# Kernel tuning notes

Measured on AMD Instinct MI355X. Metric: run time of the kernel, lower is better.

Reference implementation:

```python
import jax, jax.numpy as jnp
import numpy as np

N = 100000      # nodes
E = 1600000     # edges
F_IN = 128
F_HID = 128
F_OUT = 40
BN_EPS = 1e-5


def gcn_layer(x, W, b, src, dst):
    # PyG GCNConv with default gcn_norm: add self-loops, symmetric deg^-1/2 norm.
    h = x @ W                                   # [N, F_out] dense transform first (F_out <= F_in friendly)
    loop = jnp.arange(N)
    s = jnp.concatenate([src, loop])            # [E+N] sources incl. self-loops
    d = jnp.concatenate([dst, loop])            # [E+N] targets incl. self-loops
    deg = jax.ops.segment_sum(jnp.ones(s.shape, dtype=h.dtype), d, num_segments=N)
    dinv = jnp.where(deg > 0, jax.lax.rsqrt(deg), jnp.zeros((), h.dtype))
    norm = dinv[s] * dinv[d]                    # [E+N]
    out = jax.ops.segment_sum(h[s] * norm[:, None], d, num_segments=N)
    return out + b


def setup_inputs() -> dict:
    key = jax.random.key(0)
    ks = jax.random.split(key, 8)
    x = jax.random.normal(ks[0], (N, F_IN), dtype=jnp.float32)
    edge_src = jax.random.randint(ks[1], (E,), 0, N)
    edge_dst = jax.random.randint(ks[2], (E,), 0, N)
    W1 = jax.random.normal(ks[3], (F_IN, F_HID), dtype=jnp.float32) * (1.0 / np.sqrt(F_IN))
    b1 = jnp.zeros((F_HID,), dtype=jnp.float32)
    gamma = jnp.ones((F_HID,), dtype=jnp.float32)
    beta = jnp.zeros((F_HID,), dtype=jnp.float32)
    W2 = jax.random.normal(ks[4], (F_HID, F_OUT), dtype=jnp.float32) * (1.0 / np.sqrt(F_HID))
    b2 = jnp.zeros((F_OUT,), dtype=jnp.float32)
    return {"x": x, "W1": W1, "b1": b1, "gamma": gamma, "beta": beta,
            "W2": W2, "b2": b2, "edge_src": edge_src, "edge_dst": edge_dst}


def reference(x, W1, b1, gamma, beta, W2, b2, edge_src, edge_dst):
    h = gcn_layer(x, W1, b1, edge_src, edge_dst)            # GCNConv 1
    mean = jnp.mean(h, axis=0)                               # BatchNorm1d (batch stats, deterministic)
    var = jnp.mean(jnp.square(h - mean), axis=0)
    h = (h - mean) * jax.lax.rsqrt(var + BN_EPS) * gamma + beta
    h = jax.nn.relu(h)                                       # ReLU; dropout is identity (eval/deterministic)
    h = gcn_layer(h, W2, b2, edge_src, edge_dst)            # GCNConv 2
    return jax.nn.log_softmax(h, axis=1)
```

## Files before the change

### kernel.cpp

```cpp
#include <hip/hip_runtime.h>
#include <cstdint>
#include <cstddef>

constexpr int N_NODES = 100000;
constexpr int N_EDGES = 1600000;
constexpr int F_IN   = 128;
constexpr int F_HID  = 128;
constexpr int F_OUT  = 40;
constexpr float BN_EPS = 1e-5f;

constexpr int NBUCK  = 196;
constexpr int ECHUNK = 4096;
constexpr int NCHUNK = (N_EDGES + ECHUNK - 1) / ECHUNK;
constexpr int BCAP   = 16384;

typedef unsigned int uint;
typedef unsigned short ushort;
typedef __attribute__((ext_vector_type(8))) short short8v;
typedef __attribute__((ext_vector_type(4))) float f32x4;

__device__ inline uint bf16_rne(float f) {
    uint u = __float_as_uint(f);
    return (u + 0x7fffu + ((u >> 16) & 1u)) >> 16;
}
__device__ inline float bf_lo(uint u) { return __uint_as_float(u << 16); }
__device__ inline float bf_hi(uint u) { return __uint_as_float(u & 0xffff0000u); }

__global__ __launch_bounds__(256) void k_wcast(const float* __restrict__ W1,
                                               const float* __restrict__ W2,
                                               ushort* __restrict__ w1b,
                                               ushort* __restrict__ w2b,
                                               int* __restrict__ gfill,
                                               float* __restrict__ bnsum,
                                               float* __restrict__ bnsq) {
    int i = blockIdx.x * 256 + threadIdx.x;
    if (i < NBUCK) gfill[i] = 0;
    if (i < 128) { bnsum[i] = 0.f; bnsq[i] = 0.f; }
    if (i < 128 * 128) {
        int n = i >> 7, k = i & 127;
        w1b[i] = (ushort)bf16_rne(W1[k * 128 + n]);
    }
    if (i < 48 * 128) {
        int c = i >> 7, k = i & 127;
        w2b[i] = (c < F_OUT) ? (ushort)bf16_rne(W2[k * F_OUT + c]) : (ushort)0;
    }
}

__global__ __launch_bounds__(256) void k_part(const int* __restrict__ src,
                                              const int* __restrict__ dst,
                                              int* __restrict__ gfill,
                                              uint* __restrict__ ebuf) {
    __shared__ uint pk[ECHUNK];
    __shared__ uint gd[ECHUNK];
    __shared__ int hist[NBUCK], loff[NBUCK], gpos[NBUCK], lfill[NBUCK];
    __shared__ int sc[256];
    int t = threadIdx.x;
    for (int i = t; i < NBUCK; i += 256) { hist[i] = 0; lfill[i] = 0; }
    __syncthreads();
    int base = blockIdx.x * ECHUNK;
    int n = min(ECHUNK, N_EDGES - base);
    for (int i = t; i < n; i += 256)
        atomicAdd(&hist[dst[base + i] >> 9], 1);
    __syncthreads();
    int c = (t < NBUCK) ? hist[t] : 0;
    sc[t] = c;
    __syncthreads();
    #pragma unroll
    for (int o = 1; o < 256; o <<= 1) {
        int v = (t >= o) ? sc[t - o] : 0;
        __syncthreads();
        sc[t] += v;
        __syncthreads();
    }
    if (t < NBUCK) {
        loff[t] = sc[t] - c;
        gpos[t] = c ? atomicAdd(&gfill[t], c) : 0;
    }
    __syncthreads();
    for (int i = t; i < n; i += 256) {
        int d = dst[base + i];
        int s2 = src[base + i];
        int b = d >> 9;
        int lp = atomicAdd(&lfill[b], 1);
        int idx = loff[b] + lp;
        int off = gpos[b] + lp;
        pk[idx] = (uint)s2 | ((uint)(d & 511) << 17);
        gd[idx] = (off < BCAP) ? (uint)(b * BCAP + off) : 0xFFFFFFFFu;
    }
    __syncthreads();
    for (int i = t; i < n; i += 256) {
        uint g = gd[i];
        if (g != 0xFFFFFFFFu) ebuf[g] = pk[i];
    }
}

__global__ __launch_bounds__(256) void k_csr(const uint* __restrict__ ebuf,
                                             const int* __restrict__ gfill,
                                             int* __restrict__ rowptr,
                                             int* __restrict__ rowend,
                                             float* __restrict__ dinv,
                                             int* __restrict__ colidx) {
    __shared__ int hist[512];
    __shared__ int lptr[512];
    int t = threadIdx.x;
    int b = blockIdx.x;
    int v0 = b << 9;
    int e0 = b * BCAP;
    int m = min(gfill[b], BCAP);
    for (int i = t; i < 512; i += 256) hist[i] = 0;
    __syncthreads();
    for (int i = t; i < m; i += 256)
        atomicAdd(&hist[ebuf[e0 + i] >> 17], 1);
    __syncthreads();
    if (t < 64) {
        int run = 0;
        #pragma unroll
        for (int j = 0; j < 8; ++j) { lptr[8 * t + j] = run; run += hist[8 * t + j]; }
        int inc = run;
        #pragma unroll
        for (int o = 1; o < 64; o <<= 1) {
            int u = __shfl_up(inc, o);
            if (t >= o) inc += u;
        }
        int excl = inc - run;
        #pragma unroll
        for (int j = 0; j < 8; ++j) lptr[8 * t + j] += excl;
    }
    __syncthreads();
    for (int i = t; i < 512; i += 256) {
        int v = v0 + i;
        if (v < N_NODES) {
            int beg = e0 + lptr[i];
            rowptr[v] = beg;
            rowend[v] = beg + hist[i];
            dinv[v] = rsqrtf((float)(hist[i] + 1));
        }
    }
    __syncthreads();
    for (int i = t; i < 512; i += 256) hist[i] = 0;
    __syncthreads();
    for (int i = t; i < m; i += 256) {
        uint p = ebuf[e0 + i];
        int lr = (int)(p >> 17);
        int lp = atomicAdd(&hist[lr], 1);
        colidx[e0 + lptr[lr] + lp] = (int)(p & 0x1FFFFu);
    }
}

__global__ __launch_bounds__(256) void k_gemm1(const float* __restrict__ x,
                                               const ushort* __restrict__ w1b,
                                               const float* __restrict__ dinv,
                                               uint* __restrict__ h1b) {
    __shared__ float sm[64 * 132];
    int wid = threadIdx.x >> 6, lane = threadIdx.x & 63;
    int li = lane & 15, kg = lane >> 4;
    int row = blockIdx.x * 64 + wid * 16 + li;
    int rc = min(row, N_NODES - 1);
    const float* xr = x + (size_t)rc * 128;
    f32x4 acc[8] = {};
    #pragma unroll
    for (int kk = 0; kk < 4; ++kk) {
        int k0 = kk * 32 + kg * 8;
        float4 xv0 = *(const float4*)(xr + k0);
        float4 xv1 = *(const float4*)(xr + k0 + 4);
        short8v a;
        a[0] = (short)bf16_rne(xv0.x); a[1] = (short)bf16_rne(xv0.y);
        a[2] = (short)bf16_rne(xv0.z); a[3] = (short)bf16_rne(xv0.w);
        a[4] = (short)bf16_rne(xv1.x); a[5] = (short)bf16_rne(xv1.y);
        a[6] = (short)bf16_rne(xv1.z); a[7] = (short)bf16_rne(xv1.w);
        #pragma unroll
        for (int n = 0; n < 8; ++n) {
            short8v b = *(const short8v*)(w1b + (n * 16 + li) * 128 + k0);
            acc[n] = __builtin_amdgcn_mfma_f32_16x16x32_bf16(a, b, acc[n], 0, 0, 0);
        }
    }
    #pragma unroll
    for (int n = 0; n < 8; ++n)
        #pragma unroll
        for (int j = 0; j < 4; ++j)
            sm[(wid * 16 + kg * 4 + j) * 132 + n * 16 + li] = acc[n][j];
    __syncthreads();
    int rr = threadIdx.x >> 2, cb = (threadIdx.x & 3) * 32;
    int grow = blockIdx.x * 64 + rr;
    if (grow < N_NODES) {
        float dv = dinv[grow];
        const float4* sp4 = (const float4*)(sm + rr * 132 + cb);
        uint4 ov[4];
        #pragma unroll
        for (int q = 0; q < 4; ++q) {
            float4 e0 = sp4[2 * q], e1 = sp4[2 * q + 1];
            ov[q].x = bf16_rne(e0.x * dv) | (bf16_rne(e0.y * dv) << 16);
            ov[q].y = bf16_rne(e0.z * dv) | (bf16_rne(e0.w * dv) << 16);
            ov[q].z = bf16_rne(e1.x * dv) | (bf16_rne(e1.y * dv) << 16);
            ov[q].w = bf16_rne(e1.z * dv) | (bf16_rne(e1.w * dv) << 16);
        }
        uint4* dst = (uint4*)(h1b + (size_t)grow * 64 + cb / 2);
        #pragma unroll
        for (int q = 0; q < 4; ++q) dst[q] = ov[q];
    }
}

__global__ __launch_bounds__(256) void k_agg1(const uint* __restrict__ h1b,
                                              const int* __restrict__ rowptr,
                                              const int* __restrict__ rowend,
                                              const int* __restrict__ colidx,
                                              const float* __restrict__ dinv,
                                              const float* __restrict__ b1,
                                              uint* __restrict__ out1b) {
    const uint4* h1b4 = (const uint4*)h1b;
    int v = __builtin_amdgcn_readfirstlane(blockIdx.x * 4 + (threadIdx.x >> 6));
    if (v >= N_NODES) return;
    int lane = threadIdx.x & 63;
    int g = lane >> 4, c = lane & 15;
    int beg = rowptr[v], end = rowend[v];
    float a0 = 0, a1 = 0, a2 = 0, a3 = 0, a4 = 0, a5 = 0, a6 = 0, a7 = 0;
    #define ACC8(u) { a0 += bf_lo(u.x); a1 += bf_hi(u.x); a2 += bf_lo(u.y); a3 += bf_hi(u.y); \
                      a4 += bf_lo(u.z); a5 += bf_hi(u.z); a6 += bf_lo(u.w); a7 += bf_hi(u.w); }
    if (g == 0) {
        uint4 us = h1b4[(size_t)v * 16 + c];
        ACC8(us);
    }
    int p = beg + g;
    for (; p + 12 < end; p += 16) {
        int s0 = colidx[p], s1 = colidx[p + 4], s2 = colidx[p + 8], s3 = colidx[p + 12];
        uint4 u0 = h1b4[(size_t)s0 * 16 + c];
        uint4 u1 = h1b4[(size_t)s1 * 16 + c];
        uint4 u2 = h1b4[(size_t)s2 * 16 + c];
        uint4 u3 = h1b4[(size_t)s3 * 16 + c];
        ACC8(u0); ACC8(u1); ACC8(u2); ACC8(u3);
    }
    for (; p < end; p += 4) {
        uint4 u = h1b4[(size_t)colidx[p] * 16 + c];
        ACC8(u);
    }
    #undef ACC8
    a0 += __shfl_xor(a0, 16); a0 += __shfl_xor(a0, 32);
    a1 += __shfl_xor(a1, 16); a1 += __shfl_xor(a1, 32);
    a2 += __shfl_xor(a2, 16); a2 += __shfl_xor(a2, 32);
    a3 += __shfl_xor(a3, 16); a3 += __shfl_xor(a3, 32);
    a4 += __shfl_xor(a4, 16); a4 += __shfl_xor(a4, 32);
    a5 += __shfl_xor(a5, 16); a5 += __shfl_xor(a5, 32);
    a6 += __shfl_xor(a6, 16); a6 += __shfl_xor(a6, 32);
    a7 += __shfl_xor(a7, 16); a7 += __shfl_xor(a7, 32);
    if (g == 0) {
        float dv = dinv[v];
        const float* bp = b1 + 8 * c;
        float o0 = fmaf(dv, a0, bp[0]), o1 = fmaf(dv, a1, bp[1]);
        float o2 = fmaf(dv, a2, bp[2]), o3 = fmaf(dv, a3, bp[3]);
        float o4 = fmaf(dv, a4, bp[4]), o5 = fmaf(dv, a5, bp[5]);
        float o6 = fmaf(dv, a6, bp[6]), o7 = fmaf(dv, a7, bp[7]);
        uint4 ov;
        ov.x = bf16_rne(o0) | (bf16_rne(o1) << 16);
        ov.y = bf16_rne(o2) | (bf16_rne(o3) << 16);
        ov.z = bf16_rne(o4) | (bf16_rne(o5) << 16);
        ov.w = bf16_rne(o6) | (bf16_rne(o7) << 16);
        *(uint4*)(out1b + (size_t)v * 64 + 4 * c) = ov;
    }
}

__global__ __launch_bounds__(256) void k_bnstats(const uint* __restrict__ out1b,
                                                 float* __restrict__ sum,
                                                 float* __restrict__ sumsq) {
    int t = threadIdx.x;
    int f = t & 63;
    int r = blockIdx.x * 4 + (t >> 6);
    float s0 = 0, ss0 = 0, s1 = 0, ss1 = 0;
    for (; r < N_NODES; r += gridDim.x * 4) {
        uint u = out1b[(size_t)r * 64 + f];
        float a = bf_lo(u), b = bf_hi(u);
        s0 += a; ss0 += a * a;
        s1 += b; ss1 += b * b;
    }
    __shared__ float ls[256][4];
    ls[t][0] = s0; ls[t][1] = ss0; ls[t][2] = s1; ls[t][3] = ss1;
    __syncthreads();
    if (t < 64) {
        float A = ls[t][0] + ls[t + 64][0] + ls[t + 128][0] + ls[t + 192][0];
        float B = ls[t][1] + ls[t + 64][1] + ls[t + 128][1] + ls[t + 192][1];
        float C = ls[t][2] + ls[t + 64][2] + ls[t + 128][2] + ls[t + 192][2];
        float D = ls[t][3] + ls[t + 64][3] + ls[t + 128][3] + ls[t + 192][3];
        atomicAdd(&sum[2 * f], A);
        atomicAdd(&sumsq[2 * f], B);
        atomicAdd(&sum[2 * f + 1], C);
        atomicAdd(&sumsq[2 * f + 1], D);
    }
}

__global__ __launch_bounds__(256) void k_gemm2(const uint* __restrict__ out1b,
                                               const ushort* __restrict__ w2b,
                                               const float* __restrict__ bnsum,
                                               const float* __restrict__ bnsq,
                                               const float* __restrict__ gamma,
                                               const float* __restrict__ beta,
                                               const float* __restrict__ dinv,
                                               uint* __restrict__ h2f) {
    __shared__ float sm[64 * 52];
    __shared__ float scs[128], shs[128];
    if (threadIdx.x < 128) {
        int f = threadIdx.x;
        float mean = bnsum[f] * (1.f / N_NODES);
        float var = bnsq[f] * (1.f / N_NODES) - mean * mean;
        float rstd = rsqrtf(var + BN_EPS);
        float sc = gamma[f] * rstd;
        scs[f] = sc;
        shs[f] = beta[f] - mean * sc;
    }
    __syncthreads();
    int wid = threadIdx.x >> 6, lane = threadIdx.x & 63;
    int li = lane & 15, kg = lane >> 4;
    int row = blockIdx.x * 64 + wid * 16 + li;
    int rc = min(row, N_NODES - 1);
    const uint* xr = out1b + (size_t)rc * 64;
    f32x4 acc[3] = {};
    #pragma unroll
    for (int kk = 0; kk < 4; ++kk) {
        int k0 = kk * 32 + kg * 8;
        uint4 uv = *(const uint4*)(xr + k0 / 2);
        float4 sc0 = *(const float4*)(scs + k0);
        float4 sc1 = *(const float4*)(scs + k0 + 4);
        float4 sh0 = *(const float4*)(shs + k0);
        float4 sh1 = *(const float4*)(shs + k0 + 4);
        float e0 = fmaxf(fmaf(bf_lo(uv.x), sc0.x, sh0.x), 0.f);
        float e1 = fmaxf(fmaf(bf_hi(uv.x), sc0.y, sh0.y), 0.f);
        float e2 = fmaxf(fmaf(bf_lo(uv.y), sc0.z, sh0.z), 0.f);
        float e3 = fmaxf(fmaf(bf_hi(uv.y), sc0.w, sh0.w), 0.f);
        float e4 = fmaxf(fmaf(bf_lo(uv.z), sc1.x, sh1.x), 0.f);
        float e5 = fmaxf(fmaf(bf_hi(uv.z), sc1.y, sh1.y), 0.f);
        float e6 = fmaxf(fmaf(bf_lo(uv.w), sc1.z, sh1.z), 0.f);
        float e7 = fmaxf(fmaf(bf_hi(uv.w), sc1.w, sh1.w), 0.f);
        short8v a;
        a[0] = (short)bf16_rne(e0); a[1] = (short)bf16_rne(e1);
        a[2] = (short)bf16_rne(e2); a[3] = (short)bf16_rne(e3);
        a[4] = (short)bf16_rne(e4); a[5] = (short)bf16_rne(e5);
        a[6] = (short)bf16_rne(e6); a[7] = (short)bf16_rne(e7);
        #pragma unroll
        for (int n = 0; n < 3; ++n) {
            short8v b = *(const short8v*)(w2b + (n * 16 + li) * 128 + k0);
            acc[n] = __builtin_amdgcn_mfma_f32_16x16x32_bf16(a, b, acc[n], 0, 0, 0);
        }
    }
    #pragma unroll
    for (int n = 0; n < 3; ++n)
        #pragma unroll
        for (int j = 0; j < 4; ++j)
            sm[(wid * 16 + kg * 4 + j) * 52 + n * 16 + li] = acc[n][j];
    __syncthreads();
    int rr = threadIdx.x;
    int grow = blockIdx.x * 64 + rr;
    if (rr < 64 && grow < N_NODES) {
        float dv = dinv[grow];
        const float* sp = sm + rr * 52;
        uint o[10];
        #pragma unroll
        for (int i = 0; i < 10; ++i) {
            int p = 0;
            p = __builtin_amdgcn_cvt_pk_fp8_f32(sp[4 * i] * dv,     sp[4 * i + 1] * dv, p, false);
            p = __builtin_amdgcn_cvt_pk_fp8_f32(sp[4 * i + 2] * dv, sp[4 * i + 3] * dv, p, true);
            o[i] = (uint)p;
        }
        uint4* dst = (uint4*)(h2f + (size_t)grow * 16);
        dst[0] = make_uint4(o[0], o[1], o[2], o[3]);
        dst[1] = make_uint4(o[4], o[5], o[6], o[7]);
        *(uint2*)(h2f + (size_t)grow * 16 + 8) = make_uint2(o[8], o[9]);
    }
}

__global__ __launch_bounds__(256) void k_agg2(const uint* __restrict__ h2f,
                                              const int* __restrict__ rowptr,
                                              const int* __restrict__ rowend,
                                              const int* __restrict__ colidx,
                                              const float* __restrict__ dinv,
                                              const float* __restrict__ b2,
                                              float* __restrict__ out) {
    __shared__ float sm[4][64][4];
    int wid = threadIdx.x >> 6;
    int v = __builtin_amdgcn_readfirstlane(blockIdx.x * 4 + wid);
    if (v >= N_NODES) return;
    int lane = threadIdx.x & 63;
    int g = lane / 10;
    int c = lane - g * 10;
    bool act = g < 6;
    int beg = rowptr[v], end = rowend[v];
    float a0 = 0, a1 = 0, a2 = 0, a3 = 0;
    #define ACC4(u) { auto lo = __builtin_amdgcn_cvt_pk_f32_fp8((int)(u), false); \
                      auto hi = __builtin_amdgcn_cvt_pk_f32_fp8((int)(u), true);  \
                      a0 += lo[0]; a1 += lo[1]; a2 += hi[0]; a3 += hi[1]; }
    if (act) {
        if (g == 0) {
            uint u = h2f[(size_t)v * 16 + c];
            ACC4(u);
        }
        int p = beg + g;
        for (; p + 18 < end; p += 24) {
            int s0 = colidx[p], s1 = colidx[p + 6], s2 = colidx[p + 12], s3 = colidx[p + 18];
            uint u0 = h2f[(size_t)s0 * 16 + c];
            uint u1 = h2f[(size_t)s1 * 16 + c];
            uint u2 = h2f[(size_t)s2 * 16 + c];
            uint u3 = h2f[(size_t)s3 * 16 + c];
            ACC4(u0); ACC4(u1); ACC4(u2); ACC4(u3);
        }
        for (; p < end; p += 6) {
            uint u = h2f[(size_t)colidx[p] * 16 + c];
            ACC4(u);
        }
    }
    #undef ACC4
    float4* slot = (float4*)&sm[wid][lane][0];
    *slot = make_float4(a0, a1, a2, a3);
    asm volatile("s_waitcnt lgkmcnt(0)" ::: "memory");
    __builtin_amdgcn_sched_barrier(0);
    float z = -1e30f;
    if (lane < F_OUT) {
        int cc = lane >> 2, jj = lane & 3;
        float s = sm[wid][cc][jj]      + sm[wid][10 + cc][jj] + sm[wid][20 + cc][jj]
                + sm[wid][30 + cc][jj] + sm[wid][40 + cc][jj] + sm[wid][50 + cc][jj];
        z = fmaf(dinv[v], s, b2[lane]);
    }
    float m = z;
    #pragma unroll
    for (int off = 32; off; off >>= 1) m = fmaxf(m, __shfl_xor(m, off));
    float e = (lane < F_OUT) ? __expf(z - m) : 0.f;
    float ssum = e;
    #pragma unroll
    for (int off = 32; off; off >>= 1) ssum += __shfl_xor(ssum, off);
    if (lane < F_OUT) out[(size_t)v * F_OUT + lane] = z - m - __logf(ssum);
}

extern "C" void kernel_launch(void* const* d_in, const int* in_sizes, int n_in,
                              void* d_out, int out_size, void* d_ws, size_t ws_size,
                              hipStream_t stream) {
    const float* x     = (const float*)d_in[0];
    const float* W1    = (const float*)d_in[1];
    const float* b1    = (const float*)d_in[2];
    const float* gamma = (const float*)d_in[3];
    const float* beta  = (const float*)d_in[4];
    const float* W2    = (const float*)d_in[5];
    const float* b2    = (const float*)d_in[6];
    const int* esrc    = (const int*)d_in[7];
    const int* edst    = (const int*)d_in[8];
    float* out         = (float*)d_out;

    char* w = (char*)d_ws;
    size_t off = 0;
    auto alloc = [&](size_t bytes) -> void* {
        void* p = w + off;
        off = (off + bytes + 255) & ~(size_t)255;
        return p;
    };
    int*   gfill  = (int*)alloc(NBUCK * 4);
    int*   rowptr = (int*)alloc(N_NODES * 4);
    int*   rowend = (int*)alloc(N_NODES * 4);
    float* dinv   = (float*)alloc(N_NODES * 4);
    int*   colidx = (int*)alloc((size_t)NBUCK * BCAP * 4);
    uint*  h1b    = (uint*)alloc((size_t)N_NODES * 64 * 4);
    uint*  out1b  = (uint*)alloc((size_t)N_NODES * 64 * 4);
    uint*  h2f    = (uint*)alloc((size_t)N_NODES * 16 * 4);
    ushort* w1b   = (ushort*)alloc(128 * 128 * 2);
    ushort* w2b   = (ushort*)alloc(48 * 128 * 2);
    float* bnsum  = (float*)alloc(128 * 4);
    float* bnsq   = (float*)alloc(128 * 4);
    uint*  ebuf   = h1b;

    (void)ws_size; (void)in_sizes; (void)n_in; (void)out_size;

    k_wcast<<<64, 256, 0, stream>>>(W1, W2, w1b, w2b, gfill, bnsum, bnsq);

    k_part <<<NCHUNK, 256, 0, stream>>>(esrc, edst, gfill, ebuf);
    k_csr  <<<NBUCK, 256, 0, stream>>>(ebuf, gfill, rowptr, rowend, dinv, colidx);

    k_gemm1<<<(N_NODES + 63) / 64, 256, 0, stream>>>(x, w1b, dinv, h1b);
    k_agg1<<<(N_NODES + 3) / 4, 256, 0, stream>>>(h1b, rowptr, rowend, colidx, dinv, b1, out1b);

    k_bnstats<<<512, 256, 0, stream>>>(out1b, bnsum, bnsq);

    k_gemm2<<<(N_NODES + 63) / 64, 256, 0, stream>>>(out1b, w2b, bnsum, bnsq, gamma, beta, dinv, h2f);
    k_agg2<<<(N_NODES + 3) / 4, 256, 0, stream>>>(h2f, rowptr, rowend, colidx, dinv, b2, out);
}
```

Measured before the change: 255.3 us.

## Widen partition/CSR blocks to 512 threads, wave-scan buckets, split agg1 launch

```diff
diff --git a/kernel.cpp b/kernel.cpp
--- a/kernel.cpp
+++ b/kernel.cpp
@@ -46,38 +46,47 @@
     }
 }
 
-__global__ __launch_bounds__(256) void k_part(const int* __restrict__ src,
+__global__ __launch_bounds__(512) void k_part(const int* __restrict__ src,
                                               const int* __restrict__ dst,
                                               int* __restrict__ gfill,
                                               uint* __restrict__ ebuf) {
     __shared__ uint pk[ECHUNK];
     __shared__ uint gd[ECHUNK];
     __shared__ int hist[NBUCK], loff[NBUCK], gpos[NBUCK], lfill[NBUCK];
-    __shared__ int sc[256];
     int t = threadIdx.x;
-    for (int i = t; i < NBUCK; i += 256) { hist[i] = 0; lfill[i] = 0; }
+    for (int i = t; i < NBUCK; i += 512) { hist[i] = 0; lfill[i] = 0; }
     __syncthreads();
     int base = blockIdx.x * ECHUNK;
     int n = min(ECHUNK, N_EDGES - base);
-    for (int i = t; i < n; i += 256)
+    for (int i = t; i < n; i += 512)
         atomicAdd(&hist[dst[base + i] >> 9], 1);
     __syncthreads();
-    int c = (t < NBUCK) ? hist[t] : 0;
-    sc[t] = c;
-    __syncthreads();
-    #pragma unroll
-    for (int o = 1; o < 256; o <<= 1) {
-        int v = (t >= o) ? sc[t - o] : 0;
-        __syncthreads();
-        sc[t] += v;
-        __syncthreads();
-    }
-    if (t < NBUCK) {
-        loff[t] = sc[t] - c;
-        gpos[t] = c ? atomicAdd(&gfill[t], c) : 0;
-    }
-    __syncthreads();
-    for (int i = t; i < n; i += 256) {
+    if (t < 64) {
+        int b0 = 4 * t;
+        int h[4];
+        #pragma unroll
+        for (int j = 0; j < 4; ++j) h[j] = (b0 + j < NBUCK) ? hist[b0 + j] : 0;
+        int run = h[0] + h[1] + h[2] + h[3];
+        int inc = run;
+        #pragma unroll
+        for (int o = 1; o < 64; o <<= 1) {
+            int u = __shfl_up(inc, o);
+            if (t >= o) inc += u;
+        }
+        int excl = inc - run;
+        int pre = 0;
+        #pragma unroll
+        for (int j = 0; j < 4; ++j) {
+            int b = b0 + j;
+            if (b < NBUCK) {
+                loff[b] = excl + pre;
+                gpos[b] = h[j] ? atomicAdd(&gfill[b], h[j]) : 0;
+            }
+            pre += h[j];
+        }
+    }
+    __syncthreads();
+    for (int i = t; i < n; i += 512) {
         int d = dst[base + i];
         int s2 = src[base + i];
         int b = d >> 9;
@@ -88,13 +97,13 @@
         gd[idx] = (off < BCAP) ? (uint)(b * BCAP + off) : 0xFFFFFFFFu;
     }
     __syncthreads();
-    for (int i = t; i < n; i += 256) {
+    for (int i = t; i < n; i += 512) {
         uint g = gd[i];
         if (g != 0xFFFFFFFFu) ebuf[g] = pk[i];
     }
 }
 
-__global__ __launch_bounds__(256) void k_csr(const uint* __restrict__ ebuf,
+__global__ __launch_bounds__(512) void k_csr(const uint* __restrict__ ebuf,
                                              const int* __restrict__ gfill,
                                              int* __restrict__ rowptr,
                                              int* __restrict__ rowend,
@@ -107,9 +116,9 @@
     int v0 = b << 9;
     int e0 = b * BCAP;
     int m = min(gfill[b], BCAP);
-    for (int i = t; i < 512; i += 256) hist[i] = 0;
-    __syncthreads();
-    for (int i = t; i < m; i += 256)
+    if (t < 512) hist[t] = 0;
+    __syncthreads();
+    for (int i = t; i < m; i += 512)
         atomicAdd(&hist[ebuf[e0 + i] >> 17], 1);
     __syncthreads();
     if (t < 64) {
@@ -127,19 +136,19 @@
         for (int j = 0; j < 8; ++j) lptr[8 * t + j] += excl;
     }
     __syncthreads();
-    for (int i = t; i < 512; i += 256) {
-        int v = v0 + i;
+    {
+        int v = v0 + t;
         if (v < N_NODES) {
-            int beg = e0 + lptr[i];
+            int beg = e0 + lptr[t];
             rowptr[v] = beg;
-            rowend[v] = beg + hist[i];
-            dinv[v] = rsqrtf((float)(hist[i] + 1));
-        }
-    }
-    __syncthreads();
-    for (int i = t; i < 512; i += 256) hist[i] = 0;
-    __syncthreads();
-    for (int i = t; i < m; i += 256) {
+            rowend[v] = beg + hist[t];
+            dinv[v] = rsqrtf((float)(hist[t] + 1));
+        }
+    }
+    __syncthreads();
+    hist[t] = 0;
+    __syncthreads();
+    for (int i = t; i < m; i += 512) {
         uint p = ebuf[e0 + i];
         int lr = (int)(p >> 17);
         int lp = atomicAdd(&hist[lr], 1);
@@ -206,9 +215,10 @@
                                               const int* __restrict__ colidx,
                                               const float* __restrict__ dinv,
                                               const float* __restrict__ b1,
-                                              uint* __restrict__ out1b) {
+                                              uint* __restrict__ out1b,
+                                              int vbase) {
     const uint4* h1b4 = (const uint4*)h1b;
-    int v = __builtin_amdgcn_readfirstlane(blockIdx.x * 4 + (threadIdx.x >> 6));
+    int v = __builtin_amdgcn_readfirstlane(vbase + blockIdx.x * 4 + (threadIdx.x >> 6));
     if (v >= N_NODES) return;
     int lane = threadIdx.x & 63;
     int g = lane >> 4, c = lane & 15;
@@ -465,11 +475,12 @@
 
     k_wcast<<<64, 256, 0, stream>>>(W1, W2, w1b, w2b, gfill, bnsum, bnsq);
 
-    k_part <<<NCHUNK, 256, 0, stream>>>(esrc, edst, gfill, ebuf);
-    k_csr  <<<NBUCK, 256, 0, stream>>>(ebuf, gfill, rowptr, rowend, dinv, colidx);
+    k_part <<<NCHUNK, 512, 0, stream>>>(esrc, edst, gfill, ebuf);
+    k_csr  <<<NBUCK, 512, 0, stream>>>(ebuf, gfill, rowptr, rowend, dinv, colidx);
 
     k_gemm1<<<(N_NODES + 63) / 64, 256, 0, stream>>>(x, w1b, dinv, h1b);
-    k_agg1<<<(N_NODES + 3) / 4, 256, 0, stream>>>(h1b, rowptr, rowend, colidx, dinv, b1, out1b);
+    k_agg1<<<12500, 256, 0, stream>>>(h1b, rowptr, rowend, colidx, dinv, b1, out1b, 0);
+    k_agg1<<<12500, 256, 0, stream>>>(h1b, rowptr, rowend, colidx, dinv, b1, out1b, 50000);
 
     k_bnstats<<<512, 256, 0, stream>>>(out1b, bnsum, bnsq);
 
```

New measurement: 271.9 us. 6.5% more time.
